# Performance work log

Measured on AMD Instinct MI355X. Metric: run time of the kernel, lower is better.

The kernel has to match this reference:

```python
import jax, jax.numpy as jnp
import numpy as np

D = 256       # input_dim == output_dim (required by residual + attn Linears)
HN = 4        # num_node_heads
HT = 4        # num_type_heads
N = 50000     # nodes per node type (A and B)
E = 300000    # edges per relation (both relations are B -> A)
R = 2         # num relations incident on dst type A
ALPHA = 0.5
SLOPE = 0.01  # torch F.leaky_relu default
EPS = 1e-9


def _normalize(x):
    # torch: x / max(norm(x, dim=1, keepdim=True), 1e-9); for 2D/last-dim feature
    n = jnp.linalg.norm(x, axis=-1, keepdims=True)
    return x / jnp.maximum(n, EPS)


def setup_inputs() -> dict:
    key = jax.random.key(0)
    ks = jax.random.split(key, 16)
    s = jnp.float32(0.05)
    return {
        "h_A": jax.random.normal(ks[0], (N, D), jnp.float32),
        "h_B": jax.random.normal(ks[1], (N, D), jnp.float32),
        "src0": jax.random.randint(ks[2], (E,), 0, N),
        "dst0": jax.random.randint(ks[3], (E,), 0, N),
        "src1": jax.random.randint(ks[4], (E,), 0, N),
        "dst1": jax.random.randint(ks[5], (E,), 0, N),
        "node_W": jax.random.normal(ks[6], (2, D, D), jnp.float32) * s,
        "node_b": jnp.zeros((2, D), jnp.float32),
        "edge_W": jax.random.normal(ks[7], (R, D, D), jnp.float32) * s,
        "edge_b": jnp.zeros((R, D), jnp.float32),
        "srcA_W": jax.random.normal(ks[8], (R, D, HN), jnp.float32) * s,
        "srcA_b": jnp.zeros((R, HN), jnp.float32),
        "dstA_W": jax.random.normal(ks[9], (R, D, HN), jnp.float32) * s,
        "dstA_b": jnp.zeros((R, HN), jnp.float32),
        "semS_W": jax.random.normal(ks[10], (R, D, HT), jnp.float32) * s,
        "semS_b": jnp.zeros((R, HT), jnp.float32),
        "semD_W": jax.random.normal(ks[11], (R, D, HT), jnp.float32) * s,
        "semD_b": jnp.zeros((R, HT), jnp.float32),
        "relA_W": jax.random.normal(ks[12], (R, D, HT), jnp.float32) * s,
        "relA_b": jnp.zeros((R, HT), jnp.float32),
        "rel_emb": jax.random.normal(ks[13], (R, D), jnp.float32) * jnp.float32(1.414),
    }


def _relation_z(h_src, h_dst, We, be, Wn, bn, Ws, bs, Wd, bd, src, dst):
    """Per-relation GAT-style message passing with DGL edge_softmax semantics."""
    hs = h_src @ We + be                    # edge_linear[e_id](h_src)  [N,D]
    hd = h_dst @ Wn + bn                    # node_linear[dst_id](h_dst) [N,D]
    a_src = hs @ Ws + bs                    # src_attn  [N,HN]
    a_dst = hd @ Wd + bd                    # dst_attn  [N,HN]
    a = jax.nn.leaky_relu(a_src[src] + a_dst[dst], SLOPE)   # u_add_v  [E,HN]
    # edge_softmax: segmented softmax over in-edges of each dst node
    m = jax.ops.segment_max(a, dst, num_segments=N)
    ex = jnp.exp(a - m[dst])
    denom = jax.ops.segment_sum(ex, dst, num_segments=N)
    w = ex / denom[dst]                     # [E,HN]
    v = hs.reshape(N, HN, D // HN)
    msg = v[src] * w[:, :, None]            # u_mul_e   [E,HN,D/HN]
    z = jax.ops.segment_sum(msg, dst, num_segments=N)       # fn.sum
    return z.reshape(N, D)


def reference(h_A, h_B, src0, dst0, src1, dst1, node_W, node_b, edge_W, edge_b,
              srcA_W, srcA_b, dstA_W, dstA_b, semS_W, semS_b, semD_W, semD_b,
              relA_W, relA_b, rel_emb):
    # Graph: relations (B -r0-> A) and (B -r1-> A); node ids: A=0, B=1.
    z0 = _relation_z(h_B, h_A, edge_W[0], edge_b[0], node_W[0], node_b[0],
                     srcA_W[0], srcA_b[0], dstA_W[0], dstA_b[0], src0, dst0)
    z1 = _relation_z(h_B, h_A, edge_W[1], edge_b[1], node_W[0], node_b[0],
                     srcA_W[1], srcA_b[1], dstA_W[1], dstA_b[1], src1, dst1)
    z_src = jnp.stack([z0, z1], axis=1)     # cross_reducer='stack' [N,R,D]

    # --- dst type A: semantic + relation attention fusion ---
    z_dst = h_A @ node_W[0] + node_b[0]
    sem = (jnp.einsum('nrd,rdh->nrh', _normalize(z_src), semS_W) + semS_b
           + jnp.einsum('nd,rdh->nrh', _normalize(z_dst), semD_W) + semD_b)  # [N,R,HT]
    sem = jax.nn.softmax(jax.nn.leaky_relu(sem, SLOPE), axis=1)
    rel = jnp.einsum('rd,rdh->rh', rel_emb, relA_W) + relA_b   # [R,HT], node-invariant
    rel = jax.nn.softmax(jax.nn.leaky_relu(rel, SLOPE), axis=0)
    attn = ALPHA * sem + (1.0 - ALPHA) * rel[None]             # [N,R,HT]

    zc = (z_src.reshape(N, R, HT, D // HT) * attn[..., None]).reshape(N, R, D).sum(axis=1)
    out_A = _normalize(jax.nn.gelu(zc + h_A, approximate=False))

    # --- node type B: no incoming edges -> fallback branch ---
    out_B = _normalize(jax.nn.gelu(h_B @ node_W[1] + node_b[1] + h_B, approximate=False))
    return jnp.stack([out_A, out_B])        # [2,N,D]
```

## Files before the change

kernel.cpp:

```cpp
#include <hip/hip_runtime.h>
#include <math.h>

#define D 256
#define HN 4
#define HT 4

typedef __bf16 bf16x8 __attribute__((ext_vector_type(8)));
typedef float  f32x16 __attribute__((ext_vector_type(16)));

__device__ __forceinline__ float lrelu(float x){ return x > 0.f ? x : 0.01f*x; }
__device__ __forceinline__ float gelu_exact(float x){ return 0.5f*x*(1.f+erff(x*0.70710678118654752f)); }

__device__ __forceinline__ float wred_sum(float v){
#pragma unroll
  for (int o = 32; o > 0; o >>= 1) v += __shfl_xor(v, o);
  return v;
}
__device__ __forceinline__ float4 wred_sum4(float4 v){
  v.x = wred_sum(v.x); v.y = wred_sum(v.y); v.z = wred_sum(v.z); v.w = wred_sum(v.w);
  return v;
}

#define ACC4(p, s, w) do { (p).x = fmaf((s),(w).x,(p).x); (p).y = fmaf((s),(w).y,(p).y); \
                           (p).z = fmaf((s),(w).z,(p).z); (p).w = fmaf((s),(w).w,(p).w); } while(0)

__global__ void wt_setup(const float* __restrict__ nodeW, const float* __restrict__ edgeW,
                         __bf16* __restrict__ WtHi, __bf16* __restrict__ WtLo)
{
  int idx = blockIdx.x*256 + threadIdx.x;
  int mat = idx >> 16;
  int e   = idx & 65535;
  int n   = e & 255;
  int k   = e >> 8;
  const float* src = (mat==0)? nodeW : (mat==1)? nodeW+65536 : (mat==2)? edgeW : edgeW+65536;
  float x = src[k*256 + n];
  __bf16 hi = (__bf16)x;
  __bf16 lo = (__bf16)(x - (float)hi);
  size_t o = (size_t)mat*65536 + (size_t)n*256 + k;
  WtHi[o] = hi;
  WtLo[o] = lo;
}

__device__ __forceinline__ void cvt8(const float4 a, const float4 b, bf16x8& h, bf16x8& l){
  float v0=a.x,v1=a.y,v2=a.z,v3=a.w,v4=b.x,v5=b.y,v6=b.z,v7=b.w;
  __bf16 t;
  t=(__bf16)v0; h[0]=t; l[0]=(__bf16)(v0-(float)t);
  t=(__bf16)v1; h[1]=t; l[1]=(__bf16)(v1-(float)t);
  t=(__bf16)v2; h[2]=t; l[2]=(__bf16)(v2-(float)t);
  t=(__bf16)v3; h[3]=t; l[3]=(__bf16)(v3-(float)t);
  t=(__bf16)v4; h[4]=t; l[4]=(__bf16)(v4-(float)t);
  t=(__bf16)v5; h[5]=t; l[5]=(__bf16)(v5-(float)t);
  t=(__bf16)v6; h[6]=t; l[6]=(__bf16)(v6-(float)t);
  t=(__bf16)v7; h[7]=t; l[7]=(__bf16)(v7-(float)t);
}

__global__ __launch_bounds__(256) void gemm_mfma4(
    const float* __restrict__ hA, const float* __restrict__ hB,
    const __bf16* __restrict__ WtHi, const __bf16* __restrict__ WtLo,
    const float* __restrict__ node_b, const float* __restrict__ edge_b,
    float* __restrict__ outA, float* __restrict__ hs0,
    float* __restrict__ hs1, float* __restrict__ outB, int M)
{
  const int z = blockIdx.z;
  const float* A    = (z==0)? hA : hB;
  const int    mat  = (z==0)? 0 : (z==1)? 2 : (z==2)? 3 : 1;
  const float* bias = (z==0)? node_b : (z==1)? edge_b : (z==2)? edge_b+256 : node_b+256;
  float*       C    = (z==0)? outA : (z==1)? hs0 : (z==2)? hs1 : outB;
  const __bf16* Wh  = WtHi + (size_t)mat*65536;
  const __bf16* Wl  = WtLo + (size_t)mat*65536;

  __shared__ __align__(16) char smem[33024];
  const int tid  = threadIdx.x;
  const int bm   = blockIdx.x * 128;
  const int bn   = blockIdx.y * 128;
  const int lane = tid & 63;
  const int wid  = tid >> 6;
  const int wm   = wid >> 1, wn = wid & 1;

  f32x16 acc[2][2] = {};

  const int sm_row = tid >> 1;
  const int sk     = (tid & 1) * 16;
  int arow = bm + sm_row; if (arow >= M) arow = M - 1;
  const float*  gA  = A  + (size_t)arow*256 + sk;
  const __bf16* gWh = Wh + (size_t)(bn + sm_row)*256 + sk;
  const __bf16* gWl = Wl + (size_t)(bn + sm_row)*256 + sk;
  const int s0  = (tid & 1) * 2;
  const int wrO = sm_row * 16;

  float4 f0,f1,f2,f3; uint4 u0,u1,u2,u3;
  f0 = *(const float4*)(gA + 0);  f1 = *(const float4*)(gA + 4);
  f2 = *(const float4*)(gA + 8);  f3 = *(const float4*)(gA + 12);
  u0 = *(const uint4*)(gWh + 0);  u1 = *(const uint4*)(gWh + 8);
  u2 = *(const uint4*)(gWl + 0);  u3 = *(const uint4*)(gWl + 8);

  for (int it = 0; it < 8; ++it) {
    bf16x8 h0,h1,l0,l1;
    cvt8(f0, f1, h0, l0);
    cvt8(f2, f3, h1, l1);
    __syncthreads();
    *(bf16x8*)(smem +         s0   *2064 + wrO) = h0;
    *(bf16x8*)(smem +        (s0+1)*2064 + wrO) = h1;
    *(bf16x8*)(smem +  8256 + s0   *2064 + wrO) = l0;
    *(bf16x8*)(smem +  8256 +(s0+1)*2064 + wrO) = l1;
    *(uint4*)(smem + 16512 + s0   *2064 + wrO) = u0;
    *(uint4*)(smem + 16512 +(s0+1)*2064 + wrO) = u1;
    *(uint4*)(smem + 24768 + s0   *2064 + wrO) = u2;
    *(uint4*)(smem + 24768 +(s0+1)*2064 + wrO) = u3;
    if (it < 7) {
      int k0 = (it+1)*32;
      f0 = *(const float4*)(gA + k0 + 0);  f1 = *(const float4*)(gA + k0 + 4);
      f2 = *(const float4*)(gA + k0 + 8);  f3 = *(const float4*)(gA + k0 + 12);
      u0 = *(const uint4*)(gWh + k0);      u1 = *(const uint4*)(gWh + k0 + 8);
      u2 = *(const uint4*)(gWl + k0);      u3 = *(const uint4*)(gWl + k0 + 8);
    }
    __syncthreads();
#pragma unroll
    for (int ks = 0; ks < 2; ++ks) {
      const int fo = (ks*2 + (lane>>5))*2064 + (lane&31)*16;
      bf16x8 aH0 = *(const bf16x8*)(smem +         fo + (wm*64    )*16);
      bf16x8 aH1 = *(const bf16x8*)(smem +         fo + (wm*64+32 )*16);
      bf16x8 aL0 = *(const bf16x8*)(smem +  8256 + fo + (wm*64    )*16);
      bf16x8 aL1 = *(const bf16x8*)(smem +  8256 + fo + (wm*64+32 )*16);
      bf16x8 bH0 = *(const bf16x8*)(smem + 16512 + fo + (wn*64    )*16);
      bf16x8 bH1 = *(const bf16x8*)(smem + 16512 + fo + (wn*64+32 )*16);
      bf16x8 bL0 = *(const bf16x8*)(smem + 24768 + fo + (wn*64    )*16);
      bf16x8 bL1 = *(const bf16x8*)(smem + 24768 + fo + (wn*64+32 )*16);
      acc[0][0] = __builtin_amdgcn_mfma_f32_32x32x16_bf16(aH0,bH0,acc[0][0],0,0,0);
      acc[0][0] = __builtin_amdgcn_mfma_f32_32x32x16_bf16(aH0,bL0,acc[0][0],0,0,0);
      acc[0][0] = __builtin_amdgcn_mfma_f32_32x32x16_bf16(aL0,bH0,acc[0][0],0,0,0);
      acc[0][1] = __builtin_amdgcn_mfma_f32_32x32x16_bf16(aH0,bH1,acc[0][1],0,0,0);
      acc[0][1] = __builtin_amdgcn_mfma_f32_32x32x16_bf16(aH0,bL1,acc[0][1],0,0,0);
      acc[0][1] = __builtin_amdgcn_mfma_f32_32x32x16_bf16(aL0,bH1,acc[0][1],0,0,0);
      acc[1][0] = __builtin_amdgcn_mfma_f32_32x32x16_bf16(aH1,bH0,acc[1][0],0,0,0);
      acc[1][0] = __builtin_amdgcn_mfma_f32_32x32x16_bf16(aH1,bL0,acc[1][0],0,0,0);
      acc[1][0] = __builtin_amdgcn_mfma_f32_32x32x16_bf16(aL1,bH0,acc[1][0],0,0,0);
      acc[1][1] = __builtin_amdgcn_mfma_f32_32x32x16_bf16(aH1,bH1,acc[1][1],0,0,0);
      acc[1][1] = __builtin_amdgcn_mfma_f32_32x32x16_bf16(aH1,bL1,acc[1][1],0,0,0);
      acc[1][1] = __builtin_amdgcn_mfma_f32_32x32x16_bf16(aL1,bH1,acc[1][1],0,0,0);
    }
  }

  const int col = bn + wn*64 + (lane&31);
#pragma unroll
  for (int fn = 0; fn < 2; ++fn) {
    float bval = bias[col + fn*32];
#pragma unroll
    for (int fm = 0; fm < 2; ++fm) {
      int rbase = bm + wm*64 + fm*32 + 4*(lane>>5);
#pragma unroll
      for (int r = 0; r < 16; ++r) {
        int row = rbase + (r&3) + 8*(r>>2);
        if (row < M) C[(size_t)row*256 + col + fn*32] = acc[fm][fn][r] + bval;
      }
    }
  }
}

__global__ __launch_bounds__(256) void attn_vec_kernel(
    const float* __restrict__ hs0, const float* __restrict__ hs1,
    const float* __restrict__ hd,
    const float* __restrict__ srcA_W, const float* __restrict__ srcA_b,
    const float* __restrict__ dstA_W, const float* __restrict__ dstA_b,
    float* __restrict__ as0, float* __restrict__ as1,
    float* __restrict__ ad0, float* __restrict__ ad1, int N)
{
  int n = blockIdx.x*4 + (threadIdx.x >> 6);
  if (n >= N) return;
  int lane = threadIdx.x & 63;
  int d0 = lane << 2;
  const float4* Ws = (const float4*)srcA_W;
  const float4* Wd = (const float4*)dstA_W;
  float4 r0 = ((const float4*)hs0)[(size_t)n*64 + lane];
  float4 r1 = ((const float4*)hs1)[(size_t)n*64 + lane];
  float4 rd = ((const float4*)hd )[(size_t)n*64 + lane];
  float4 p0 = make_float4(0,0,0,0), p1 = make_float4(0,0,0,0);
  float4 q0 = make_float4(0,0,0,0), q1 = make_float4(0,0,0,0);
  float4 w;
  w = Ws[d0+0]; ACC4(p0, r0.x, w);
  w = Ws[d0+1]; ACC4(p0, r0.y, w);
  w = Ws[d0+2]; ACC4(p0, r0.z, w);
  w = Ws[d0+3]; ACC4(p0, r0.w, w);
  w = Ws[256+d0+0]; ACC4(p1, r1.x, w);
  w = Ws[256+d0+1]; ACC4(p1, r1.y, w);
  w = Ws[256+d0+2]; ACC4(p1, r1.z, w);
  w = Ws[256+d0+3]; ACC4(p1, r1.w, w);
  w = Wd[d0+0]; ACC4(q0, rd.x, w);
  w = Wd[d0+1]; ACC4(q0, rd.y, w);
  w = Wd[d0+2]; ACC4(q0, rd.z, w);
  w = Wd[d0+3]; ACC4(q0, rd.w, w);
  w = Wd[256+d0+0]; ACC4(q1, rd.x, w);
  w = Wd[256+d0+1]; ACC4(q1, rd.y, w);
  w = Wd[256+d0+2]; ACC4(q1, rd.z, w);
  w = Wd[256+d0+3]; ACC4(q1, rd.w, w);
  p0 = wred_sum4(p0); p1 = wred_sum4(p1); q0 = wred_sum4(q0); q1 = wred_sum4(q1);
  if (lane == 0) {
    float4 b;
    b = *(const float4*)(srcA_b + 0);
    ((float4*)as0)[n] = make_float4(p0.x+b.x, p0.y+b.y, p0.z+b.z, p0.w+b.w);
    b = *(const float4*)(srcA_b + 4);
    ((float4*)as1)[n] = make_float4(p1.x+b.x, p1.y+b.y, p1.z+b.z, p1.w+b.w);
    b = *(const float4*)(dstA_b + 0);
    ((float4*)ad0)[n] = make_float4(q0.x+b.x, q0.y+b.y, q0.z+b.z, q0.w+b.w);
    b = *(const float4*)(dstA_b + 4);
    ((float4*)ad1)[n] = make_float4(q1.x+b.x, q1.y+b.y, q1.z+b.z, q1.w+b.w);
  }
}

__global__ void rel_kernel(const float* __restrict__ rel_emb, const float* __restrict__ relA_W,
                           const float* __restrict__ relA_b, float* __restrict__ rel_out)
{
  int t = threadIdx.x;
  if (t < 8) {
    int r = t >> 2, h = t & 3;
    float s = relA_b[r*4+h];
    for (int d = 0; d < 256; ++d)
      s = fmaf(rel_emb[r*256+d], relA_W[(size_t)(r*256+d)*4+h], s);
    s = lrelu(s);
    float other = __shfl_xor(s, 4);
    float mm = fmaxf(s, other);
    float e  = expf(s - mm), eo = expf(other - mm);
    rel_out[r*4+h] = 0.5f * e / (e + eo);
  }
}

__global__ void zero_int(int* p, int n){
  int i = blockIdx.x*blockDim.x + threadIdx.x;
  if (i < n) p[i] = 0;
}

__global__ void hist_kernel(const int* __restrict__ dst0, const int* __restrict__ dst1,
                            int* c0, int* c1, int E){
  int e = blockIdx.x*256 + threadIdx.x;
  if (e < E) { atomicAdd(&c0[dst0[e]], 1); atomicAdd(&c1[dst1[e]], 1); }
}

__global__ __launch_bounds__(1024) void scan1(const int* __restrict__ cnt0, const int* __restrict__ cnt1,
                                              int* __restrict__ rp0, int* __restrict__ rp1,
                                              int* __restrict__ part0, int* __restrict__ part1, int n){
  const int* cnt = blockIdx.y ? cnt1 : cnt0;
  int* excl = blockIdx.y ? rp1 : rp0;
  int* part = blockIdx.y ? part1 : part0;
  __shared__ int sm[1024];
  int tid = threadIdx.x;
  int gid = blockIdx.x*1024 + tid;
  int v = (gid < n) ? cnt[gid] : 0;
  sm[tid] = v; __syncthreads();
  for (int off = 1; off < 1024; off <<= 1){
    int t = sm[tid];
    if (tid >= off) t += sm[tid-off];
    __syncthreads();
    sm[tid] = t; __syncthreads();
  }
  if (gid < n) excl[gid] = sm[tid] - v;
  if (tid == 1023) part[blockIdx.x] = sm[1023];
}

__global__ void scan2(int* part0, int* part1, int nchunk, int* tot0, int* tot1){
  if (threadIdx.x == 0 && blockIdx.x == 0){
    int run = 0;
    for (int i = 0; i < nchunk; ++i){ int t = part0[i]; part0[i] = run; run += t; }
    *tot0 = run;
    run = 0;
    for (int i = 0; i < nchunk; ++i){ int t = part1[i]; part1[i] = run; run += t; }
    *tot1 = run;
  }
}

__global__ __launch_bounds__(1024) void scan3(int* __restrict__ rp0, int* __restrict__ rp1,
                                              int* __restrict__ cur0, int* __restrict__ cur1,
                                              const int* __restrict__ part0, const int* __restrict__ part1, int n){
  int* rp  = blockIdx.y ? rp1 : rp0;
  int* cur = blockIdx.y ? cur1 : cur0;
  const int* part = blockIdx.y ? part1 : part0;
  int gid = blockIdx.x*1024 + threadIdx.x;
  if (gid < n){ int v = rp[gid] + part[blockIdx.x]; rp[gid] = v; cur[gid] = v; }
}

__global__ void scatter_kernel(const int* __restrict__ src0, const int* __restrict__ dst0,
                               int* cur0, int* __restrict__ csr0,
                               const int* __restrict__ src1, const int* __restrict__ dst1,
                               int* cur1, int* __restrict__ csr1, int E){
  int e = blockIdx.x*256 + threadIdx.x;
  if (e < E){
    int p = atomicAdd(&cur0[dst0[e]], 1); csr0[p] = src0[e];
    p = atomicAdd(&cur1[dst1[e]], 1); csr1[p] = src1[e];
  }
}

__device__ __forceinline__ void sm2(float s0, float s1, float r0, float r1, float& o0, float& o1){
  float mm = fmaxf(s0, s1);
  float e0 = expf(s0-mm), e1 = expf(s1-mm);
  float inv = 1.f/(e0+e1);
  o0 = fmaf(0.5f*e0, inv, r0);
  o1 = fmaf(0.5f*e1, inv, r1);
}

__global__ __launch_bounds__(256) void aggregate_fused2(
    const int* __restrict__ rp0, const int* __restrict__ csr0,
    const float* __restrict__ as0, const float* __restrict__ ad0,
    const float* __restrict__ hs0,
    const int* __restrict__ rp1, const int* __restrict__ csr1,
    const float* __restrict__ as1, const float* __restrict__ ad1,
    const float* __restrict__ hs1,
    float* __restrict__ hd_io, const float* __restrict__ hA,
    const float* __restrict__ semS_W, const float* __restrict__ semS_b,
    const float* __restrict__ semD_W, const float* __restrict__ semD_b,
    const float* __restrict__ relw, int N)
{
  __shared__ float4 a1_lds[2][64];
  const int tid    = threadIdx.x;
  const int lane   = tid & 63;
  const int wid    = tid >> 6;
  const int locn   = wid >> 1;
  const int rel    = wid & 1;
  const int n      = blockIdx.x*2 + locn;
  const int h      = lane >> 4;
  const bool active = (n < N);

  float4 acc = make_float4(0.f,0.f,0.f,0.f);
  if (active) {
    const int*   rp  = rel ? rp1  : rp0;
    const int*   csr = rel ? csr1 : csr0;
    const float* as  = rel ? as1  : as0;
    const float* ad  = rel ? ad1  : ad0;
    const float* hs  = rel ? hs1  : hs0;
    int start = rp[n];
    int cnt   = rp[n+1] - start;
    if (cnt > 0) {
      float adh = ad[(size_t)n*4 + h];
      const float4* hsv = (const float4*)hs;
      float ssum = 0.f;
      int i = 0;
      for (; i+4 <= cnt; i += 4) {
        int s0 = csr[start+i], s1 = csr[start+i+1], s2 = csr[start+i+2], s3 = csr[start+i+3];
        float w0 = __expf(lrelu(as[(size_t)s0*4+h] + adh));
        float w1 = __expf(lrelu(as[(size_t)s1*4+h] + adh));
        float w2 = __expf(lrelu(as[(size_t)s2*4+h] + adh));
        float w3 = __expf(lrelu(as[(size_t)s3*4+h] + adh));
        float4 v0 = hsv[(size_t)s0*64 + lane];
        float4 v1 = hsv[(size_t)s1*64 + lane];
        float4 v2 = hsv[(size_t)s2*64 + lane];
        float4 v3 = hsv[(size_t)s3*64 + lane];
        acc.x = fmaf(v0.x,w0,acc.x); acc.y = fmaf(v0.y,w0,acc.y);
        acc.z = fmaf(v0.z,w0,acc.z); acc.w = fmaf(v0.w,w0,acc.w);
        acc.x = fmaf(v1.x,w1,acc.x); acc.y = fmaf(v1.y,w1,acc.y);
        acc.z = fmaf(v1.z,w1,acc.z); acc.w = fmaf(v1.w,w1,acc.w);
        acc.x = fmaf(v2.x,w2,acc.x); acc.y = fmaf(v2.y,w2,acc.y);
        acc.z = fmaf(v2.z,w2,acc.z); acc.w = fmaf(v2.w,w2,acc.w);
        acc.x = fmaf(v3.x,w3,acc.x); acc.y = fmaf(v3.y,w3,acc.y);
        acc.z = fmaf(v3.z,w3,acc.z); acc.w = fmaf(v3.w,w3,acc.w);
        ssum += w0 + w1 + w2 + w3;
      }
      for (; i < cnt; ++i) {
        int s = csr[start+i];
        float wv = __expf(lrelu(as[(size_t)s*4+h] + adh));
        float4 v = hsv[(size_t)s*64 + lane];
        acc.x = fmaf(v.x,wv,acc.x); acc.y = fmaf(v.y,wv,acc.y);
        acc.z = fmaf(v.z,wv,acc.z); acc.w = fmaf(v.w,wv,acc.w);
        ssum += wv;
      }
      float inv = 1.f / ssum;
      acc.x *= inv; acc.y *= inv; acc.z *= inv; acc.w *= inv;
    }
  }
  if (rel == 1) a1_lds[locn][lane] = acc;
  __syncthreads();
  if (rel == 1 || !active) return;

  float4 a0 = acc;
  float4 a1 = a1_lds[locn][lane];
  int d0 = lane << 2;
  float4 ad = ((float4*)hd_io)[(size_t)n*64 + lane];
  float4 ha = ((const float4*)hA)[(size_t)n*64 + lane];
  float nz0 = wred_sum(a0.x*a0.x + a0.y*a0.y + a0.z*a0.z + a0.w*a0.w);
  float nz1 = wred_sum(a1.x*a1.x + a1.y*a1.y + a1.z*a1.z + a1.w*a1.w);
  float nzd = wred_sum(ad.x*ad.x + ad.y*ad.y + ad.z*ad.z + ad.w*ad.w);
  float i0  = 1.f / fmaxf(sqrtf(nz0), 1e-9f);
  float i1  = 1.f / fmaxf(sqrtf(nz1), 1e-9f);
  float idn = 1.f / fmaxf(sqrtf(nzd), 1e-9f);
  const float4* WS = (const float4*)semS_W;
  const float4* WD = (const float4*)semD_W;
  float4 p0 = make_float4(0,0,0,0), p1 = make_float4(0,0,0,0);
  float4 q0 = make_float4(0,0,0,0), q1 = make_float4(0,0,0,0);
  float4 w;
  w = WS[d0+0]; ACC4(p0, a0.x, w);
  w = WS[d0+1]; ACC4(p0, a0.y, w);
  w = WS[d0+2]; ACC4(p0, a0.z, w);
  w = WS[d0+3]; ACC4(p0, a0.w, w);
  w = WS[256+d0+0]; ACC4(p1, a1.x, w);
  w = WS[256+d0+1]; ACC4(p1, a1.y, w);
  w = WS[256+d0+2]; ACC4(p1, a1.z, w);
  w = WS[256+d0+3]; ACC4(p1, a1.w, w);
  w = WD[d0+0]; ACC4(q0, ad.x, w);
  w = WD[d0+1]; ACC4(q0, ad.y, w);
  w = WD[d0+2]; ACC4(q0, ad.z, w);
  w = WD[d0+3]; ACC4(q0, ad.w, w);
  w = WD[256+d0+0]; ACC4(q1, ad.x, w);
  w = WD[256+d0+1]; ACC4(q1, ad.y, w);
  w = WD[256+d0+2]; ACC4(q1, ad.z, w);
  w = WD[256+d0+3]; ACC4(q1, ad.w, w);
  p0 = wred_sum4(p0); p1 = wred_sum4(p1); q0 = wred_sum4(q0); q1 = wred_sum4(q1);
  float4 sb0 = *(const float4*)(semS_b + 0);
  float4 sb1 = *(const float4*)(semS_b + 4);
  float4 db0 = *(const float4*)(semD_b + 0);
  float4 db1 = *(const float4*)(semD_b + 4);
  float4 s0, s1;
  s0.x = lrelu(p0.x*i0 + sb0.x + q0.x*idn + db0.x);
  s0.y = lrelu(p0.y*i0 + sb0.y + q0.y*idn + db0.y);
  s0.z = lrelu(p0.z*i0 + sb0.z + q0.z*idn + db0.z);
  s0.w = lrelu(p0.w*i0 + sb0.w + q0.w*idn + db0.w);
  s1.x = lrelu(p1.x*i1 + sb1.x + q1.x*idn + db1.x);
  s1.y = lrelu(p1.y*i1 + sb1.y + q1.y*idn + db1.y);
  s1.z = lrelu(p1.z*i1 + sb1.z + q1.z*idn + db1.z);
  s1.w = lrelu(p1.w*i1 + sb1.w + q1.w*idn + db1.w);
  float4 at0, at1;
  sm2(s0.x, s1.x, relw[0], relw[4], at0.x, at1.x);
  sm2(s0.y, s1.y, relw[1], relw[5], at0.y, at1.y);
  sm2(s0.z, s1.z, relw[2], relw[6], at0.z, at1.z);
  sm2(s0.w, s1.w, relw[3], relw[7], at0.w, at1.w);
  float w0 = h==0 ? at0.x : h==1 ? at0.y : h==2 ? at0.z : at0.w;
  float w1 = h==0 ? at1.x : h==1 ? at1.y : h==2 ? at1.z : at1.w;
  float4 x;
  x.x = fmaf(a0.x, w0, fmaf(a1.x, w1, ha.x));
  x.y = fmaf(a0.y, w0, fmaf(a1.y, w1, ha.y));
  x.z = fmaf(a0.z, w0, fmaf(a1.z, w1, ha.z));
  x.w = fmaf(a0.w, w0, fmaf(a1.w, w1, ha.w));
  float4 g;
  g.x = gelu_exact(x.x); g.y = gelu_exact(x.y); g.z = gelu_exact(x.z); g.w = gelu_exact(x.w);
  float ng = wred_sum(g.x*g.x + g.y*g.y + g.z*g.z + g.w*g.w);
  float inv = 1.f / fmaxf(sqrtf(ng), 1e-9f);
  g.x *= inv; g.y *= inv; g.z *= inv; g.w *= inv;
  ((float4*)hd_io)[(size_t)n*64 + lane] = g;
}

__global__ __launch_bounds__(256) void fusionB_kernel(float* __restrict__ outB,
                                                      const float* __restrict__ hB, int N)
{
  int n = blockIdx.x*4 + (threadIdx.x >> 6);
  if (n >= N) return;
  int lane = threadIdx.x & 63;
  float4 x = ((float4*)outB)[(size_t)n*64 + lane];
  float4 b = ((const float4*)hB)[(size_t)n*64 + lane];
  x.x += b.x; x.y += b.y; x.z += b.z; x.w += b.w;
  float4 g;
  g.x = gelu_exact(x.x); g.y = gelu_exact(x.y); g.z = gelu_exact(x.z); g.w = gelu_exact(x.w);
  float ng = wred_sum(g.x*g.x + g.y*g.y + g.z*g.z + g.w*g.w);
  float inv = 1.f / fmaxf(sqrtf(ng), 1e-9f);
  g.x *= inv; g.y *= inv; g.z *= inv; g.w *= inv;
  ((float4*)outB)[(size_t)n*64 + lane] = g;
}

extern "C" void kernel_launch(void* const* d_in, const int* in_sizes, int n_in,
                              void* d_out, int out_size, void* d_ws, size_t ws_size,
                              hipStream_t stream)
{
  const float* hA     = (const float*)d_in[0];
  const float* hB     = (const float*)d_in[1];
  const int*   src0   = (const int*)d_in[2];
  const int*   dst0   = (const int*)d_in[3];
  const int*   src1   = (const int*)d_in[4];
  const int*   dst1   = (const int*)d_in[5];
  const float* node_W = (const float*)d_in[6];
  const float* node_b = (const float*)d_in[7];
  const float* edge_W = (const float*)d_in[8];
  const float* edge_b = (const float*)d_in[9];
  const float* srcA_W = (const float*)d_in[10];
  const float* srcA_b = (const float*)d_in[11];
  const float* dstA_W = (const float*)d_in[12];
  const float* dstA_b = (const float*)d_in[13];
  const float* semS_W = (const float*)d_in[14];
  const float* semS_b = (const float*)d_in[15];
  const float* semD_W = (const float*)d_in[16];
  const float* semD_b = (const float*)d_in[17];
  const float* relA_W = (const float*)d_in[18];
  const float* relA_b = (const float*)d_in[19];
  const float* rel_emb= (const float*)d_in[20];

  const int N = in_sizes[0] / D;
  const int E = in_sizes[2];

  float* out  = (float*)d_out;
  float* outA = out;
  float* outB = out + (size_t)N*D;

  float* w = (float*)d_ws;
  float* hs0  = w; w += (size_t)N*D;
  float* hs1  = w; w += (size_t)N*D;
  float* as0  = w; w += (size_t)N*HN;
  float* as1  = w; w += (size_t)N*HN;
  float* ad0  = w; w += (size_t)N*HN;
  float* ad1  = w; w += (size_t)N*HN;
  float* relw = w; w += 16;
  __bf16* WtHi = (__bf16*)w; w += 131072;
  __bf16* WtLo = (__bf16*)w; w += 131072;
  int* ip   = (int*)w;
  int* cnt0 = ip; ip += N;
  int* cnt1 = ip; ip += N;
  int* rp0  = ip; ip += N+1;
  int* rp1  = ip; ip += N+1;
  int* cur0 = ip; ip += N;
  int* cur1 = ip; ip += N;
  int* part0= ip; ip += 256;
  int* part1= ip; ip += 256;
  int* csr0 = ip; ip += E;
  int* csr1 = ip; ip += E;

  const int nwb = (N + 3) / 4;

  wt_setup<<<1024, 256, 0, stream>>>(node_W, edge_W, WtHi, WtLo);

  dim3 ggrid((N + 127)/128, 2, 4);
  gemm_mfma4<<<ggrid, 256, 0, stream>>>(hA, hB, WtHi, WtLo, node_b, edge_b,
                                        outA, hs0, hs1, outB, N);

  attn_vec_kernel<<<nwb, 256, 0, stream>>>(hs0, hs1, outA, srcA_W, srcA_b, dstA_W, dstA_b,
                                           as0, as1, ad0, ad1, N);
  rel_kernel<<<1, 64, 0, stream>>>(rel_emb, relA_W, relA_b, relw);

  zero_int<<<(2*N + 255)/256, 256, 0, stream>>>(cnt0, 2*N);
  hist_kernel<<<(E + 255)/256, 256, 0, stream>>>(dst0, dst1, cnt0, cnt1, E);
  const int nchunk = (N + 1023)/1024;
  dim3 sgrid(nchunk, 2);
  scan1<<<sgrid, 1024, 0, stream>>>(cnt0, cnt1, rp0, rp1, part0, part1, N);
  scan2<<<1, 64, 0, stream>>>(part0, part1, nchunk, rp0 + N, rp1 + N);
  scan3<<<sgrid, 1024, 0, stream>>>(rp0, rp1, cur0, cur1, part0, part1, N);
  scatter_kernel<<<(E + 255)/256, 256, 0, stream>>>(src0, dst0, cur0, csr0,
                                                    src1, dst1, cur1, csr1, E);

  aggregate_fused2<<<(N + 1)/2, 256, 0, stream>>>(rp0, csr0, as0, ad0, hs0,
                                                  rp1, csr1, as1, ad1, hs1,
                                                  outA, hA, semS_W, semS_b, semD_W, semD_b,
                                                  relw, N);

  fusionB_kernel<<<nwb, 256, 0, stream>>>(outB, hB, N);
}
```

Before: 629.6 us.

## Widen GEMM tile to full N with 512 threads and direct-to-LDS weight loads

The GEMM block now covers all 256 output columns with 8 waves instead of 128 columns with 4 waves. Each A row-tile is therefore loaded and split into bf16 hi/lo parts once rather than twice. Weight tiles are streamed straight into LDS with global_load_lds from a new k-chunked layout that wt_setup writes as vectorized 8-element stores. The change uses more LDS per block (about 48KB) and may lower occupancy, in exchange for halving A-side global traffic and conversion work.

```diff
diff --git a/kernel.cpp b/kernel.cpp
--- a/kernel.cpp
+++ b/kernel.cpp
@@ -27,18 +27,23 @@
 __global__ void wt_setup(const float* __restrict__ nodeW, const float* __restrict__ edgeW,
                          __bf16* __restrict__ WtHi, __bf16* __restrict__ WtLo)
 {
-  int idx = blockIdx.x*256 + threadIdx.x;
-  int mat = idx >> 16;
-  int e   = idx & 65535;
-  int n   = e & 255;
-  int k   = e >> 8;
+  int t = blockIdx.x*256 + threadIdx.x;
+  int mat = t >> 13;
+  int r   = t & 8191;
+  int ks  = r >> 8;
+  int n   = r & 255;
   const float* src = (mat==0)? nodeW : (mat==1)? nodeW+65536 : (mat==2)? edgeW : edgeW+65536;
-  float x = src[k*256 + n];
-  __bf16 hi = (__bf16)x;
-  __bf16 lo = (__bf16)(x - (float)hi);
-  size_t o = (size_t)mat*65536 + (size_t)n*256 + k;
-  WtHi[o] = hi;
-  WtLo[o] = lo;
+  bf16x8 hi, lo;
+#pragma unroll
+  for (int j = 0; j < 8; ++j){
+    float x = src[(size_t)(ks*8 + j)*256 + n];
+    __bf16 h = (__bf16)x;
+    hi[j] = h;
+    lo[j] = (__bf16)(x - (float)h);
+  }
+  size_t o = (size_t)mat*65536 + ((size_t)ks*256 + n)*8;
+  *(bf16x8*)(WtHi + o) = hi;
+  *(bf16x8*)(WtLo + o) = lo;
 }
 
 __device__ __forceinline__ void cvt8(const float4 a, const float4 b, bf16x8& h, bf16x8& l){
@@ -54,14 +59,16 @@
   t=(__bf16)v7; h[7]=t; l[7]=(__bf16)(v7-(float)t);
 }
 
-__global__ __launch_bounds__(256) void gemm_mfma4(
+#define MFMA32 __builtin_amdgcn_mfma_f32_32x32x16_bf16
+
+__global__ __launch_bounds__(512, 4) void gemm_mfma4(
     const float* __restrict__ hA, const float* __restrict__ hB,
     const __bf16* __restrict__ WtHi, const __bf16* __restrict__ WtLo,
     const float* __restrict__ node_b, const float* __restrict__ edge_b,
     float* __restrict__ outA, float* __restrict__ hs0,
     float* __restrict__ hs1, float* __restrict__ outB, int M)
 {
-  const int z = blockIdx.z;
+  const int z = blockIdx.y;
   const float* A    = (z==0)? hA : hB;
   const int    mat  = (z==0)? 0 : (z==1)? 2 : (z==2)? 3 : 1;
   const float* bias = (z==0)? node_b : (z==1)? edge_b : (z==2)? edge_b+256 : node_b+256;
@@ -69,89 +76,88 @@
   const __bf16* Wh  = WtHi + (size_t)mat*65536;
   const __bf16* Wl  = WtLo + (size_t)mat*65536;
 
-  __shared__ __align__(16) char smem[33024];
+  __shared__ __align__(16) char smem[49408];
   const int tid  = threadIdx.x;
   const int bm   = blockIdx.x * 128;
-  const int bn   = blockIdx.y * 128;
   const int lane = tid & 63;
   const int wid  = tid >> 6;
-  const int wm   = wid >> 1, wn = wid & 1;
+  const int wm   = wid >> 2;
+  const int wn   = wid & 3;
 
   f32x16 acc[2][2] = {};
 
-  const int sm_row = tid >> 1;
-  const int sk     = (tid & 1) * 16;
-  int arow = bm + sm_row; if (arow >= M) arow = M - 1;
-  const float*  gA  = A  + (size_t)arow*256 + sk;
-  const __bf16* gWh = Wh + (size_t)(bn + sm_row)*256 + sk;
-  const __bf16* gWl = Wl + (size_t)(bn + sm_row)*256 + sk;
-  const int s0  = (tid & 1) * 2;
-  const int wrO = sm_row * 16;
-
-  float4 f0,f1,f2,f3; uint4 u0,u1,u2,u3;
-  f0 = *(const float4*)(gA + 0);  f1 = *(const float4*)(gA + 4);
-  f2 = *(const float4*)(gA + 8);  f3 = *(const float4*)(gA + 12);
-  u0 = *(const uint4*)(gWh + 0);  u1 = *(const uint4*)(gWh + 8);
-  u2 = *(const uint4*)(gWl + 0);  u3 = *(const uint4*)(gWl + 8);
+  const int a_row  = tid >> 2;
+  const int a_slot = tid & 3;
+  int arow = bm + a_row; if (arow >= M) arow = M - 1;
+  const float* gA = A + (size_t)arow*256 + a_slot*8;
+  const int a_wr = a_slot*2064 + a_row*16;
+
+  float4 f0, f1;
+  f0 = *(const float4*)(gA + 0);
+  f1 = *(const float4*)(gA + 4);
 
   for (int it = 0; it < 8; ++it) {
-    bf16x8 h0,h1,l0,l1;
-    cvt8(f0, f1, h0, l0);
-    cvt8(f2, f3, h1, l1);
+    bf16x8 hh, ll;
+    cvt8(f0, f1, hh, ll);
     __syncthreads();
-    *(bf16x8*)(smem +         s0   *2064 + wrO) = h0;
-    *(bf16x8*)(smem +        (s0+1)*2064 + wrO) = h1;
-    *(bf16x8*)(smem +  8256 + s0   *2064 + wrO) = l0;
-    *(bf16x8*)(smem +  8256 +(s0+1)*2064 + wrO) = l1;
-    *(uint4*)(smem + 16512 + s0   *2064 + wrO) = u0;
-    *(uint4*)(smem + 16512 +(s0+1)*2064 + wrO) = u1;
-    *(uint4*)(smem + 24768 + s0   *2064 + wrO) = u2;
-    *(uint4*)(smem + 24768 +(s0+1)*2064 + wrO) = u3;
-    if (it < 7) {
-      int k0 = (it+1)*32;
-      f0 = *(const float4*)(gA + k0 + 0);  f1 = *(const float4*)(gA + k0 + 4);
-      f2 = *(const float4*)(gA + k0 + 8);  f3 = *(const float4*)(gA + k0 + 12);
-      u0 = *(const uint4*)(gWh + k0);      u1 = *(const uint4*)(gWh + k0 + 8);
-      u2 = *(const uint4*)(gWl + k0);      u3 = *(const uint4*)(gWl + k0 + 8);
+    *(bf16x8*)(smem +         a_wr) = hh;
+    *(bf16x8*)(smem +  8256 + a_wr) = ll;
+#pragma unroll
+    for (int c = 0; c < 4; ++c) {
+      int ch     = wid*4 + c;
+      int region = ch >> 4;
+      int slot   = (ch >> 2) & 3;
+      int half   = ch & 3;
+      const __bf16* gsrc = (region ? Wl : Wh)
+                         + ((size_t)((it*4 + slot)*256 + half*64)*8) + (size_t)lane*8;
+      char* ldst = smem + 16512 + region*16448 + slot*4112 + half*1024;
+      __builtin_amdgcn_global_load_lds(
+          (const __attribute__((address_space(1))) void*)gsrc,
+          (__attribute__((address_space(3))) void*)ldst, 16, 0, 0);
     }
     __syncthreads();
+    if (it < 7) {
+      f0 = *(const float4*)(gA + (it+1)*32 + 0);
+      f1 = *(const float4*)(gA + (it+1)*32 + 4);
+    }
 #pragma unroll
     for (int ks = 0; ks < 2; ++ks) {
-      const int fo = (ks*2 + (lane>>5))*2064 + (lane&31)*16;
-      bf16x8 aH0 = *(const bf16x8*)(smem +         fo + (wm*64    )*16);
-      bf16x8 aH1 = *(const bf16x8*)(smem +         fo + (wm*64+32 )*16);
-      bf16x8 aL0 = *(const bf16x8*)(smem +  8256 + fo + (wm*64    )*16);
-      bf16x8 aL1 = *(const bf16x8*)(smem +  8256 + fo + (wm*64+32 )*16);
-      bf16x8 bH0 = *(const bf16x8*)(smem + 16512 + fo + (wn*64    )*16);
-      bf16x8 bH1 = *(const bf16x8*)(smem + 16512 + fo + (wn*64+32 )*16);
-      bf16x8 bL0 = *(const bf16x8*)(smem + 24768 + fo + (wn*64    )*16);
-      bf16x8 bL1 = *(const bf16x8*)(smem + 24768 + fo + (wn*64+32 )*16);
-      acc[0][0] = __builtin_amdgcn_mfma_f32_32x32x16_bf16(aH0,bH0,acc[0][0],0,0,0);
-      acc[0][0] = __builtin_amdgcn_mfma_f32_32x32x16_bf16(aH0,bL0,acc[0][0],0,0,0);
-      acc[0][0] = __builtin_amdgcn_mfma_f32_32x32x16_bf16(aL0,bH0,acc[0][0],0,0,0);
-      acc[0][1] = __builtin_amdgcn_mfma_f32_32x32x16_bf16(aH0,bH1,acc[0][1],0,0,0);
-      acc[0][1] = __builtin_amdgcn_mfma_f32_32x32x16_bf16(aH0,bL1,acc[0][1],0,0,0);
-      acc[0][1] = __builtin_amdgcn_mfma_f32_32x32x16_bf16(aL0,bH1,acc[0][1],0,0,0);
-      acc[1][0] = __builtin_amdgcn_mfma_f32_32x32x16_bf16(aH1,bH0,acc[1][0],0,0,0);
-      acc[1][0] = __builtin_amdgcn_mfma_f32_32x32x16_bf16(aH1,bL0,acc[1][0],0,0,0);
-      acc[1][0] = __builtin_amdgcn_mfma_f32_32x32x16_bf16(aL1,bH0,acc[1][0],0,0,0);
-      acc[1][1] = __builtin_amdgcn_mfma_f32_32x32x16_bf16(aH1,bH1,acc[1][1],0,0,0);
-      acc[1][1] = __builtin_amdgcn_mfma_f32_32x32x16_bf16(aH1,bL1,acc[1][1],0,0,0);
-      acc[1][1] = __builtin_amdgcn_mfma_f32_32x32x16_bf16(aL1,bH1,acc[1][1],0,0,0);
+      const int sA =         (ks*2 + (lane>>5))*2064 + (lane&31)*16;
+      const int sW = 16512 + (ks*2 + (lane>>5))*4112 + (lane&31)*16;
+      bf16x8 aH0 = *(const bf16x8*)(smem +        sA + (wm*64    )*16);
+      bf16x8 aH1 = *(const bf16x8*)(smem +        sA + (wm*64+32 )*16);
+      bf16x8 aL0 = *(const bf16x8*)(smem + 8256 + sA + (wm*64    )*16);
+      bf16x8 aL1 = *(const bf16x8*)(smem + 8256 + sA + (wm*64+32 )*16);
+      bf16x8 bH0 = *(const bf16x8*)(smem +         sW + (wn*64    )*16);
+      bf16x8 bH1 = *(const bf16x8*)(smem +         sW + (wn*64+32 )*16);
+      bf16x8 bL0 = *(const bf16x8*)(smem + 16448 + sW + (wn*64    )*16);
+      bf16x8 bL1 = *(const bf16x8*)(smem + 16448 + sW + (wn*64+32 )*16);
+      acc[0][0] = MFMA32(aH0,bH0,acc[0][0],0,0,0);
+      acc[0][0] = MFMA32(aH0,bL0,acc[0][0],0,0,0);
+      acc[0][0] = MFMA32(aL0,bH0,acc[0][0],0,0,0);
+      acc[0][1] = MFMA32(aH0,bH1,acc[0][1],0,0,0);
+      acc[0][1] = MFMA32(aH0,bL1,acc[0][1],0,0,0);
+      acc[0][1] = MFMA32(aL0,bH1,acc[0][1],0,0,0);
+      acc[1][0] = MFMA32(aH1,bH0,acc[1][0],0,0,0);
+      acc[1][0] = MFMA32(aH1,bL0,acc[1][0],0,0,0);
+      acc[1][0] = MFMA32(aL1,bH0,acc[1][0],0,0,0);
+      acc[1][1] = MFMA32(aH1,bH1,acc[1][1],0,0,0);
+      acc[1][1] = MFMA32(aH1,bL1,acc[1][1],0,0,0);
+      acc[1][1] = MFMA32(aL1,bH1,acc[1][1],0,0,0);
     }
   }
 
-  const int col = bn + wn*64 + (lane&31);
 #pragma unroll
   for (int fn = 0; fn < 2; ++fn) {
-    float bval = bias[col + fn*32];
+    const int col = wn*64 + fn*32 + (lane&31);
+    float bval = bias[col];
 #pragma unroll
     for (int fm = 0; fm < 2; ++fm) {
       int rbase = bm + wm*64 + fm*32 + 4*(lane>>5);
 #pragma unroll
       for (int r = 0; r < 16; ++r) {
         int row = rbase + (r&3) + 8*(r>>2);
-        if (row < M) C[(size_t)row*256 + col + fn*32] = acc[fm][fn][r] + bval;
+        if (row < M) C[(size_t)row*256 + col] = acc[fm][fn][r] + bval;
       }
     }
   }
@@ -508,10 +514,10 @@
 
   const int nwb = (N + 3) / 4;
 
-  wt_setup<<<1024, 256, 0, stream>>>(node_W, edge_W, WtHi, WtLo);
-
-  dim3 ggrid((N + 127)/128, 2, 4);
-  gemm_mfma4<<<ggrid, 256, 0, stream>>>(hA, hB, WtHi, WtLo, node_b, edge_b,
+  wt_setup<<<128, 256, 0, stream>>>(node_W, edge_W, WtHi, WtLo);
+
+  dim3 ggrid((N + 127)/128, 4);
+  gemm_mfma4<<<ggrid, 512, 0, stream>>>(hA, hB, WtHi, WtLo, node_b, edge_b,
                                         outA, hs0, hs1, outB, N);
 
   attn_vec_kernel<<<nwb, 256, 0, stream>>>(hs0, hs1, outA, srcA_W, srcA_b, dstA_W, dstA_b,
```

Measured after the change: 596.7 us. -5.2%, faster.
